# Kernel optimization log

Hardware: AMD Instinct MI355X
Metric: run time of the kernel (lower is better)

The kernel has to match this reference:

```python
import jax, jax.numpy as jnp
import numpy as np

GRID = 14    # grid_size[0]
PATCH = 16   # patch_size[0]

def setup_inputs() -> dict:
    key = jax.random.key(0)
    x = jax.random.normal(key, (32, 96, 224, 224), dtype=jnp.float32)
    return {"x": x}

def reference(x):
    # x: [B, C, H, W] with H = W = GRID*PATCH
    B, C, H, W = x.shape
    g, p = GRID, PATCH
    # [B, C, gi, pi, gj, pj]
    t = x.reshape(B, C, g, p, g, p)
    # L2 norm over (C, gi, gj) for each intra-patch offset (pi, pj) -> [B, p, p]
    sq = jnp.sum(t * t, axis=(1, 2, 4))
    norms = jnp.sqrt(sq)
    # argmax over flattened (pi, pj), pj fastest -> matches torch reshape order
    idx = jnp.argmax(norms.reshape(B, p * p), axis=1)
    si = idx // p  # row shift
    sj = idx % p   # col shift
    # circular pad + translate-by-(si,sj) + crop == circular roll by (-si, -sj)
    out = jax.vmap(lambda xi, a, b: jnp.roll(xi, (-a, -b), axis=(1, 2)))(x, si, sj)
    return out
```

## Files before the change

kernel.cpp:

```cpp
#include <hip/hip_runtime.h>

#define GRIDSZ 14
#define PATCH  16
#define H      224
#define W      224
#define B      32
#define C      96


__global__ void zero_norms_kernel(float* __restrict__ nbuf) {
    int i = blockIdx.x * blockDim.x + threadIdx.x;
    nbuf[i] = 0.0f;
}

__global__ void norms_kernel(const float* __restrict__ x, float* __restrict__ nbuf) {
    int bi    = blockIdx.x;
    int slice = bi & 3;
    int pi    = (bi >> 2) & 15;
    int b     = bi >> 6;
    int wave  = threadIdx.x >> 6;
    int lane  = threadIdx.x & 63;

    __shared__ float bins[16];
    if (threadIdx.x < 16) bins[threadIdx.x] = 0.0f;
    __syncthreads();

    float a0 = 0.f, a1 = 0.f, a2 = 0.f, a3 = 0.f;
    if (lane < 56) {
        const size_t batchOff = (size_t)b * C * H * W;
        int c  = slice * 24;
        int gi = wave;
        for (int it = 0; it < 84; ++it) {
            int h = gi * PATCH + pi;
            const float4* row = (const float4*)(x + batchOff + ((size_t)c * H + h) * W);
            float4 v = row[lane];
            a0 += v.x * v.x;
            a1 += v.y * v.y;
            a2 += v.z * v.z;
            a3 += v.w * v.w;
            gi += 4;
            if (gi >= 14) { gi -= 14; c += 1; }
        }
        int base = (lane & 3) << 2;
        atomicAdd(&bins[base + 0], a0);
        atomicAdd(&bins[base + 1], a1);
        atomicAdd(&bins[base + 2], a2);
        atomicAdd(&bins[base + 3], a3);
    }
    __syncthreads();
    if (threadIdx.x < 16)
        atomicAdd(&nbuf[(b * 16 + pi) * 16 + threadIdx.x], bins[threadIdx.x]);
}

__global__ void argmax_kernel(const float* __restrict__ nbuf, int2* __restrict__ shifts) {
    int b = blockIdx.x;
    int t = threadIdx.x;
    float v = -1.0f;
    int idx = 0;
    for (int r = 0; r < 4; ++r) {
        int i = r * 64 + t;
        float u = nbuf[b * 256 + i];
        if (u > v) { v = u; idx = i; }
    }
    for (int off = 32; off > 0; off >>= 1) {
        float ov = __shfl_down(v, off);
        int   oi = __shfl_down(idx, off);
        if (ov > v || (ov == v && oi < idx)) { v = ov; idx = oi; }
    }
    if (t == 0) shifts[b] = make_int2(idx >> 4, idx & 15);
}

__global__ void roll_kernel(const float* __restrict__ x, float* __restrict__ out,
                            const int2* __restrict__ shifts) {
    int blk   = blockIdx.x;
    int b     = blk / 672;
    int chunk = blk % 672;
    int wave  = threadIdx.x >> 6;
    int lane  = threadIdx.x & 63;

    int2 s = shifts[b];
    int si = s.x, sj = s.y;

    __shared__ __align__(16) float buf[4][224];
    const size_t batchOff = (size_t)b * C * H * W;

    for (int it = 0; it < 8; ++it) {
        int rowInBatch = chunk * 32 + it * 4 + wave;
        int c = rowInBatch / H;
        int h = rowInBatch - c * H;
        int sh = h + si; if (sh >= H) sh -= H;

        const float4* src = (const float4*)(x + batchOff + ((size_t)c * H + sh) * W);
        if (lane < 56) {
            float4 v = src[lane];
            *(float4*)&buf[wave][lane * 4] = v;
        }
        __syncthreads();
        if (lane < 56) {
            int w0 = lane * 4 + sj;
            int i0 = w0;     if (i0 >= W) i0 -= W;
            int i1 = w0 + 1; if (i1 >= W) i1 -= W;
            int i2 = w0 + 2; if (i2 >= W) i2 -= W;
            int i3 = w0 + 3; if (i3 >= W) i3 -= W;
            float4 o;
            o.x = buf[wave][i0];
            o.y = buf[wave][i1];
            o.z = buf[wave][i2];
            o.w = buf[wave][i3];
            float4* dst = (float4*)(out + batchOff + (size_t)rowInBatch * W);
            dst[lane] = o;
        }
        __syncthreads();
    }
}

extern "C" void kernel_launch(void* const* d_in, const int* in_sizes, int n_in,
                              void* d_out, int out_size, void* d_ws, size_t ws_size,
                              hipStream_t stream) {
    const float* x = (const float*)d_in[0];
    float* outp = (float*)d_out;
    float* nbuf = (float*)d_ws;
    int2* shifts = (int2*)((char*)d_ws + 8192 * sizeof(float));

    zero_norms_kernel<<<32, 256, 0, stream>>>(nbuf);
    norms_kernel<<<2048, 256, 0, stream>>>(x, nbuf);
    argmax_kernel<<<32, 64, 0, stream>>>(nbuf, shifts);
    roll_kernel<<<21504, 256, 0, stream>>>(x, outp, shifts);
}
```

Before: 364.1 us.

## Replace LDS roll with register shuffles, split norm partials, drop zero kernel

The roll kernel now reads a rotated float4 index per lane and builds the sub-float4 shift with cross-lane shuffles specialised by sj mod 4. This removes the shared-memory staging and the two block barriers per row. The norms kernel uses two independent accumulator streams to expose more memory parallelism. When the workspace is large enough it writes per-slice partials directly instead of using atomics, which removes the zero-init launch, and argmax sums the four slices. The added risks are workspace-size dependence and the shuffle correctness at lanes near 56.

```diff
diff --git a/kernel.cpp b/kernel.cpp
--- a/kernel.cpp
+++ b/kernel.cpp
@@ -1,11 +1,9 @@
 #include <hip/hip_runtime.h>
 
-#define GRIDSZ 14
-#define PATCH  16
-#define H      224
-#define W      224
-#define B      32
-#define C      96
+#define H 224
+#define W 224
+#define B 32
+#define C 96
 
 
 __global__ void zero_norms_kernel(float* __restrict__ nbuf) {
@@ -13,11 +11,11 @@
     nbuf[i] = 0.0f;
 }
 
+template<int DIRECT>
 __global__ void norms_kernel(const float* __restrict__ x, float* __restrict__ nbuf) {
-    int bi    = blockIdx.x;
-    int slice = bi & 3;
-    int pi    = (bi >> 2) & 15;
-    int b     = bi >> 6;
+    int pi    = blockIdx.x >> 2;
+    int slice = blockIdx.x & 3;
+    int b     = blockIdx.y;
     int wave  = threadIdx.x >> 6;
     int lane  = threadIdx.x & 63;
 
@@ -25,33 +23,39 @@
     if (threadIdx.x < 16) bins[threadIdx.x] = 0.0f;
     __syncthreads();
 
-    float a0 = 0.f, a1 = 0.f, a2 = 0.f, a3 = 0.f;
     if (lane < 56) {
-        const size_t batchOff = (size_t)b * C * H * W;
+        const float* base = x + (size_t)b * C * H * W;
         int c  = slice * 24;
         int gi = wave;
-        for (int it = 0; it < 84; ++it) {
-            int h = gi * PATCH + pi;
-            const float4* row = (const float4*)(x + batchOff + ((size_t)c * H + h) * W);
-            float4 v = row[lane];
-            a0 += v.x * v.x;
-            a1 += v.y * v.y;
-            a2 += v.z * v.z;
-            a3 += v.w * v.w;
-            gi += 4;
-            if (gi >= 14) { gi -= 14; c += 1; }
+        float a0=0.f,a1=0.f,a2=0.f,a3=0.f;
+        float b0=0.f,b1=0.f,b2=0.f,b3=0.f;
+        #pragma unroll 2
+        for (int it = 0; it < 42; ++it) {
+            const float4* rowA = (const float4*)(base + ((size_t)c * H + gi * 16 + pi) * W);
+            const float4* rowB = rowA + (size_t)12 * H * W / 4;
+            float4 va = rowA[lane];
+            float4 vb = rowB[lane];
+            a0 += va.x * va.x; a1 += va.y * va.y; a2 += va.z * va.z; a3 += va.w * va.w;
+            b0 += vb.x * vb.x; b1 += vb.y * vb.y; b2 += vb.z * vb.z; b3 += vb.w * vb.w;
+            gi += 4; if (gi >= 14) { gi -= 14; c += 1; }
         }
-        int base = (lane & 3) << 2;
-        atomicAdd(&bins[base + 0], a0);
-        atomicAdd(&bins[base + 1], a1);
-        atomicAdd(&bins[base + 2], a2);
-        atomicAdd(&bins[base + 3], a3);
+        a0 += b0; a1 += b1; a2 += b2; a3 += b3;
+        int bse = (lane & 3) << 2;
+        atomicAdd(&bins[bse + 0], a0);
+        atomicAdd(&bins[bse + 1], a1);
+        atomicAdd(&bins[bse + 2], a2);
+        atomicAdd(&bins[bse + 3], a3);
     }
     __syncthreads();
-    if (threadIdx.x < 16)
-        atomicAdd(&nbuf[(b * 16 + pi) * 16 + threadIdx.x], bins[threadIdx.x]);
+    if (threadIdx.x < 16) {
+        if (DIRECT)
+            nbuf[((slice * B + b) * 16 + pi) * 16 + threadIdx.x] = bins[threadIdx.x];
+        else
+            atomicAdd(&nbuf[(b * 16 + pi) * 16 + threadIdx.x], bins[threadIdx.x]);
+    }
 }
 
+template<int DIRECT>
 __global__ void argmax_kernel(const float* __restrict__ nbuf, int2* __restrict__ shifts) {
     int b = blockIdx.x;
     int t = threadIdx.x;
@@ -59,7 +63,13 @@
     int idx = 0;
     for (int r = 0; r < 4; ++r) {
         int i = r * 64 + t;
-        float u = nbuf[b * 256 + i];
+        float u;
+        if (DIRECT) {
+            int o = b * 256 + i;
+            u = nbuf[o] + nbuf[8192 + o] + nbuf[16384 + o] + nbuf[24576 + o];
+        } else {
+            u = nbuf[b * 256 + i];
+        }
         if (u > v) { v = u; idx = i; }
     }
     for (int off = 32; off > 0; off >>= 1) {
@@ -70,47 +80,60 @@
     if (t == 0) shifts[b] = make_int2(idx >> 4, idx & 15);
 }
 
+template<int R>
+__device__ __forceinline__ void roll_body(const float* __restrict__ xb,
+                                          float* __restrict__ ob,
+                                          int c0, int h0, int sh0,
+                                          int q, int lane) {
+    int v = lane + q;  if (v >= 56) v -= 56;
+    int nl = lane + 1; if (nl >= 56) nl = 0;
+    int sh = sh0;
+    #pragma unroll
+    for (int it = 0; it < 8; ++it) {
+        int h = h0 + it * 4;
+        const float4* srow = (const float4*)(xb + ((size_t)c0 * H + sh) * W);
+        float4*       drow = (float4*)      (ob + ((size_t)c0 * H + h)  * W);
+        float4 a = srow[v];
+        float4 o;
+        if (R == 0) {
+            o = a;
+        } else {
+            float nx = __shfl(a.x, nl);
+            float ny = (R >= 2) ? __shfl(a.y, nl) : 0.0f;
+            float nz = (R == 3) ? __shfl(a.z, nl) : 0.0f;
+            if (R == 1) { o.x = a.y; o.y = a.z; o.z = a.w; o.w = nx; }
+            if (R == 2) { o.x = a.z; o.y = a.w; o.z = nx;  o.w = ny; }
+            if (R == 3) { o.x = a.w; o.y = nx;  o.z = ny;  o.w = nz; }
+        }
+        drow[lane] = o;
+        sh += 4; if (sh >= H) sh -= H;
+    }
+}
+
 __global__ void roll_kernel(const float* __restrict__ x, float* __restrict__ out,
                             const int2* __restrict__ shifts) {
-    int blk   = blockIdx.x;
-    int b     = blk / 672;
-    int chunk = blk % 672;
+    int b     = blockIdx.y;
+    int chunk = blockIdx.x;
     int wave  = threadIdx.x >> 6;
     int lane  = threadIdx.x & 63;
+    if (lane >= 56) return;
 
     int2 s = shifts[b];
     int si = s.x, sj = s.y;
+    int q = sj >> 2, r = sj & 3;
 
-    __shared__ __align__(16) float buf[4][224];
-    const size_t batchOff = (size_t)b * C * H * W;
+    int c0 = chunk / 7;
+    int h0 = (chunk % 7) * 32 + wave;
+    int sh0 = h0 + si; if (sh0 >= H) sh0 -= H;
 
-    for (int it = 0; it < 8; ++it) {
-        int rowInBatch = chunk * 32 + it * 4 + wave;
-        int c = rowInBatch / H;
-        int h = rowInBatch - c * H;
-        int sh = h + si; if (sh >= H) sh -= H;
+    const float* xb = x   + (size_t)b * C * H * W;
+    float*       ob = out + (size_t)b * C * H * W;
 
-        const float4* src = (const float4*)(x + batchOff + ((size_t)c * H + sh) * W);
-        if (lane < 56) {
-            float4 v = src[lane];
-            *(float4*)&buf[wave][lane * 4] = v;
-        }
-        __syncthreads();
-        if (lane < 56) {
-            int w0 = lane * 4 + sj;
-            int i0 = w0;     if (i0 >= W) i0 -= W;
-            int i1 = w0 + 1; if (i1 >= W) i1 -= W;
-            int i2 = w0 + 2; if (i2 >= W) i2 -= W;
-            int i3 = w0 + 3; if (i3 >= W) i3 -= W;
-            float4 o;
-            o.x = buf[wave][i0];
-            o.y = buf[wave][i1];
-            o.z = buf[wave][i2];
-            o.w = buf[wave][i3];
-            float4* dst = (float4*)(out + batchOff + (size_t)rowInBatch * W);
-            dst[lane] = o;
-        }
-        __syncthreads();
+    switch (r) {
+        case 0: roll_body<0>(xb, ob, c0, h0, sh0, q, lane); break;
+        case 1: roll_body<1>(xb, ob, c0, h0, sh0, q, lane); break;
+        case 2: roll_body<2>(xb, ob, c0, h0, sh0, q, lane); break;
+        default: roll_body<3>(xb, ob, c0, h0, sh0, q, lane); break;
     }
 }
 
@@ -119,11 +142,20 @@
                               hipStream_t stream) {
     const float* x = (const float*)d_in[0];
     float* outp = (float*)d_out;
-    float* nbuf = (float*)d_ws;
-    int2* shifts = (int2*)((char*)d_ws + 8192 * sizeof(float));
 
-    zero_norms_kernel<<<32, 256, 0, stream>>>(nbuf);
-    norms_kernel<<<2048, 256, 0, stream>>>(x, nbuf);
-    argmax_kernel<<<32, 64, 0, stream>>>(nbuf, shifts);
-    roll_kernel<<<21504, 256, 0, stream>>>(x, outp, shifts);
+    const size_t directBytes = (size_t)4 * B * 256 * sizeof(float);
+    if (ws_size >= directBytes + 256) {
+        float* nbuf  = (float*)d_ws;
+        int2* shifts = (int2*)((char*)d_ws + directBytes);
+        norms_kernel<1><<<dim3(64, 32), 256, 0, stream>>>(x, nbuf);
+        argmax_kernel<1><<<32, 64, 0, stream>>>(nbuf, shifts);
+        roll_kernel<<<dim3(672, 32), 256, 0, stream>>>(x, outp, shifts);
+    } else {
+        float* nbuf  = (float*)d_ws;
+        int2* shifts = (int2*)((char*)d_ws + 8192 * sizeof(float));
+        zero_norms_kernel<<<32, 256, 0, stream>>>(nbuf);
+        norms_kernel<0><<<dim3(64, 32), 256, 0, stream>>>(x, nbuf);
+        argmax_kernel<0><<<32, 64, 0, stream>>>(nbuf, shifts);
+        roll_kernel<<<dim3(672, 32), 256, 0, stream>>>(x, outp, shifts);
+    }
 }
```

After: 353.2 us. 1.03x faster.
